# Kernel optimization log

Hardware: AMD Instinct MI355X
Metric: run time of the kernel (lower is better)

The kernel has to match this reference:

```python
import jax, jax.numpy as jnp
import numpy as np
import math

V, BS, D, L, H = 50257, 1024, 768, 12, 4
DH = D // H  # 192
B, T = 4, 1024


def setup_inputs() -> dict:
    key = jax.random.key(0)
    ks = jax.random.split(key, 18)
    s = 0.02
    inp = {
        "x": jax.random.randint(ks[0], (B, T), 0, V),
        "tok_emb": jax.random.normal(ks[1], (V, D), jnp.float32) * s,
        "pos_emb": jax.random.normal(ks[2], (BS, D), jnp.float32) * s,
        "ln1_s": jnp.ones((L, D), jnp.float32),
        "ln1_b": jnp.zeros((L, D), jnp.float32),
        "qkv_w": jax.random.normal(ks[3], (L, D, 3 * D), jnp.float32) * s,
        "qkv_b": jnp.zeros((L, 3 * D), jnp.float32),
        "ln2_s": jnp.ones((L, D), jnp.float32),
        "ln2_b": jnp.zeros((L, D), jnp.float32),
        "fc_w": jax.random.normal(ks[4], (L, D, 4 * D), jnp.float32) * s,
        "fc_b": jnp.zeros((L, 4 * D), jnp.float32),
        "proj_w": jax.random.normal(ks[5], (L, 4 * D, D), jnp.float32) * s,
        "proj_b": jnp.zeros((L, D), jnp.float32),
        "lnf_s": jnp.ones((D,), jnp.float32),
        "lnf_b": jnp.zeros((D,), jnp.float32),
        "head_w": jax.random.normal(ks[6], (D, V), jnp.float32) * s,
        "head_b": jnp.zeros((V,), jnp.float32),
    }
    return inp


def _ln(x, scale, shift):
    m = x.mean(-1, keepdims=True)
    v = jnp.mean((x - m) ** 2, axis=-1, keepdims=True)
    return (x - m) * jax.lax.rsqrt(v + 1e-5) * scale + shift


def _forward(x, tok_emb, pos_emb, ln1_s, ln1_b, qkv_w, qkv_b, ln2_s, ln2_b,
             fc_w, fc_b, proj_w, proj_b, lnf_s, lnf_b, head_w, head_b):
    Bx, Tx = x.shape
    h = tok_emb[x] + pos_emb[:Tx]  # [B,T,D]
    causal = jnp.tril(jnp.ones((Tx, Tx), bool))
    scale = 1.0 / math.sqrt(DH)

    def block(h, p):
        s1, b1, wq, bq, s2, b2, wf, bf, wp, bp = p
        # attention (no output projection, faithful to source)
        ln1 = _ln(h, s1, b1)
        qkv = ln1 @ wq + bq  # [B,T,3D]
        q, k, v = jnp.split(qkv, 3, axis=-1)
        q = q.reshape(Bx, Tx, H, DH)
        k = k.reshape(Bx, Tx, H, DH)
        v = v.reshape(Bx, Tx, H, DH)
        att = jnp.einsum('bthd,bshd->bhts', q, k) * scale
        att = jnp.where(causal, att, -jnp.inf)
        att = jax.nn.softmax(att, axis=-1)
        y = jnp.einsum('bhts,bshd->bthd', att, v).reshape(Bx, Tx, D)
        h = h + y
        # MLP (ReLU, despite attr named gelu in source)
        ln2 = _ln(h, s2, b2)
        m = jax.nn.relu(ln2 @ wf + bf) @ wp + bp
        return h + m, None

    h, _ = jax.lax.scan(block, h,
                        (ln1_s, ln1_b, qkv_w, qkv_b, ln2_s, ln2_b,
                         fc_w, fc_b, proj_w, proj_b))
    h = _ln(h, lnf_s, lnf_b)
    return h @ head_w + head_b  # [B,T,V]


def reference(x, tok_emb, pos_emb, ln1_s, ln1_b, qkv_w, qkv_b, ln2_s, ln2_b,
              fc_w, fc_b, proj_w, proj_b, lnf_s, lnf_b, head_w, head_b):
    return _forward(x, tok_emb, pos_emb, ln1_s, ln1_b, qkv_w, qkv_b,
                    ln2_s, ln2_b, fc_w, fc_b, proj_w, proj_b,
                    lnf_s, lnf_b, head_w, head_b)
```

## Files before the change

### kernel.cpp

```cpp
#include <hip/hip_runtime.h>
#include <stdint.h>

#define D_MODEL 768
#define NHEAD 4
#define DHEAD 192
#define SEQ 1024
#define NLAYER 12
#define NTOK 4096
#define NVOCAB 50257

typedef __attribute__((ext_vector_type(4))) float f32x4;
typedef __attribute__((ext_vector_type(4))) int i32x4;
typedef __attribute__((ext_vector_type(4))) unsigned short u16x4;

__device__ __forceinline__ unsigned short f2bf(float f) {
  unsigned u = __builtin_bit_cast(unsigned, f);
  u += 0x7FFFu + ((u >> 16) & 1u);
  return (unsigned short)(u >> 16);
}

#define GLDS(src, dst)                                                   \
  __builtin_amdgcn_global_load_lds(                                      \
      (const __attribute__((address_space(1))) void*)(src),              \
      (__attribute__((address_space(3))) void*)(dst), 16, 0, 0)

__global__ __launch_bounds__(256) void embed_kernel(
    const int* __restrict__ x, const float* __restrict__ tok,
    const float* __restrict__ pos, float* __restrict__ h) {
  int row = blockIdx.x;
  int t = row & (SEQ - 1);
  int id = x[row];
  const float* tp = tok + (long)id * D_MODEL;
  const float* pp = pos + (long)t * D_MODEL;
  float* hp = h + (long)row * D_MODEL;
  for (int j = threadIdx.x; j < D_MODEL; j += 256)
    hp[j] = tp[j] + pp[j];
}

__global__ __launch_bounds__(256) void ln_kernel(
    const float* __restrict__ h, const float* __restrict__ sc,
    const float* __restrict__ sh, unsigned short* __restrict__ out) {
  __shared__ float red[4];
  int row = blockIdx.x;
  const float* x = h + (long)row * D_MODEL;
  int tid = threadIdx.x;
  float v0 = x[tid], v1 = x[tid + 256], v2 = x[tid + 512];
  float s = v0 + v1 + v2;
  for (int o = 32; o > 0; o >>= 1) s += __shfl_xor(s, o);
  if ((tid & 63) == 0) red[tid >> 6] = s;
  __syncthreads();
  float mean = (red[0] + red[1] + red[2] + red[3]) * (1.0f / D_MODEL);
  __syncthreads();
  float d0 = v0 - mean, d1 = v1 - mean, d2 = v2 - mean;
  float q = d0 * d0 + d1 * d1 + d2 * d2;
  for (int o = 32; o > 0; o >>= 1) q += __shfl_xor(q, o);
  if ((tid & 63) == 0) red[tid >> 6] = q;
  __syncthreads();
  float var = (red[0] + red[1] + red[2] + red[3]) * (1.0f / D_MODEL);
  float r = rsqrtf(var + 1e-5f);
  unsigned short* op = out + (long)row * D_MODEL;
  op[tid]       = f2bf(d0 * r * sc[tid]       + sh[tid]);
  op[tid + 256] = f2bf(d1 * r * sc[tid + 256] + sh[tid + 256]);
  op[tid + 512] = f2bf(d2 * r * sc[tid + 512] + sh[tid + 512]);
}

__global__ __launch_bounds__(256) void wtrans3_kernel(
    const float* __restrict__ qw, const float* __restrict__ fw,
    const float* __restrict__ pw, unsigned short* __restrict__ tq,
    unsigned short* __restrict__ tf, unsigned short* __restrict__ tp) {
  __shared__ unsigned short tile[32][33];
  int bid = blockIdx.x;
  const float* src; unsigned short* dst; int K, N, nb;
  if (bid < 1728)               { src = qw; dst = tq; K = 768;  N = 2304; nb = 72; }
  else if ((bid -= 1728) < 2304){ src = fw; dst = tf; K = 768;  N = 3072; nb = 96; }
  else { bid -= 2304;             src = pw; dst = tp; K = 3072; N = 768;  nb = 24; }
  int n0 = (bid % nb) * 32, k0 = (bid / nb) * 32;
  int tx = threadIdx.x & 31, ty = threadIdx.x >> 5;
  #pragma unroll
  for (int i = 0; i < 4; ++i) {
    int k = k0 + ty + i * 8;
    tile[ty + i * 8][tx] = f2bf(src[(long)k * N + n0 + tx]);
  }
  __syncthreads();
  #pragma unroll
  for (int i = 0; i < 4; ++i) {
    int nn = n0 + ty + i * 8;
    dst[(long)nn * K + k0 + tx] = tile[tx][ty + i * 8];
  }
}

__global__ __launch_bounds__(256) void wtrans_kernel(
    const float* __restrict__ w, unsigned short* __restrict__ wt, int K, int N) {
  __shared__ unsigned short tile[32][33];
  int n0 = blockIdx.x * 32, k0 = blockIdx.y * 32;
  int tx = threadIdx.x, ty = threadIdx.y;
  int n = n0 + tx; if (n >= N) n = N - 1;
  #pragma unroll
  for (int i = 0; i < 4; ++i) {
    int k = k0 + ty + i * 8;
    tile[ty + i * 8][tx] = f2bf(w[(long)k * N + n]);
  }
  __syncthreads();
  #pragma unroll
  for (int i = 0; i < 4; ++i) {
    int nn = n0 + ty + i * 8;
    if (nn < N) wt[(long)nn * K + k0 + tx] = tile[tx][ty + i * 8];
  }
}

__global__ __launch_bounds__(256) void vt_kernel(
    const unsigned short* __restrict__ qkv, unsigned short* __restrict__ vt) {
  __shared__ unsigned short tile[32][33];
  int bh = blockIdx.z, b = bh >> 2, hh = bh & 3;
  int t0 = blockIdx.x * 32, f0 = blockIdx.y * 32;
  int tx = threadIdx.x, ty = threadIdx.y;
  const unsigned short* src = qkv + (long)b * SEQ * 2304 + 2 * D_MODEL + hh * DHEAD;
  #pragma unroll
  for (int i = 0; i < 4; ++i) {
    int t = t0 + ty + i * 8;
    tile[ty + i * 8][tx] = src[(long)t * 2304 + f0 + tx];
  }
  __syncthreads();
  unsigned short* dst = vt + (long)bh * DHEAD * SEQ;
  #pragma unroll
  for (int i = 0; i < 4; ++i) {
    int f = f0 + ty + i * 8;
    dst[(long)f * SEQ + t0 + tx] = tile[tx][ty + i * 8];
  }
}

__global__ __launch_bounds__(256) void softmax_kernel(
    const float* __restrict__ S, unsigned short* __restrict__ P) {
  __shared__ float red[4];
  long rid = blockIdx.x;
  int q = (int)(rid & (SEQ - 1));
  int tid = threadIdx.x;
  int i0 = tid * 4;
  f32x4 v;
  if (i0 <= q) {
    v = *(const f32x4*)(S + rid * SEQ + i0);
  } else {
    v = f32x4{-3.0e38f, -3.0e38f, -3.0e38f, -3.0e38f};
  }
  float m = -3.0e38f;
  #pragma unroll
  for (int j = 0; j < 4; ++j) {
    if (i0 + j > q) v[j] = -3.0e38f;
    m = fmaxf(m, v[j]);
  }
  for (int o = 32; o > 0; o >>= 1) m = fmaxf(m, __shfl_xor(m, o));
  if ((tid & 63) == 0) red[tid >> 6] = m;
  __syncthreads();
  m = fmaxf(fmaxf(red[0], red[1]), fmaxf(red[2], red[3]));
  __syncthreads();
  float e[4];
  float sum = 0.f;
  #pragma unroll
  for (int j = 0; j < 4; ++j) {
    e[j] = (i0 + j > q) ? 0.f : __expf(v[j] - m);
    sum += e[j];
  }
  for (int o = 32; o > 0; o >>= 1) sum += __shfl_xor(sum, o);
  if ((tid & 63) == 0) red[tid >> 6] = sum;
  __syncthreads();
  float inv = 1.0f / (red[0] + red[1] + red[2] + red[3]);
  if ((i0 >> 7) <= (q >> 7)) {
    u16x4 out;
    #pragma unroll
    for (int j = 0; j < 4; ++j) out[j] = f2bf(e[j] * inv);
    *(u16x4*)(P + rid * SEQ + i0) = out;
  }
}

#define BM 128
#define BN 128
#define BKK 32

template<int MODE>
__global__ __launch_bounds__(256) void gemm_kernel(
    const unsigned short* __restrict__ A, int lda,
    const unsigned short* __restrict__ B, int ldb,
    const float* __restrict__ bias,
    void* __restrict__ Cv, int ldc,
    int M, int N, int K,
    int NI, long sAo, long sAi, long sBo, long sBi,
    long sCo, long sCi, float alpha, int causal, int mblocks) {
  __shared__ __align__(16) unsigned short As[2][BM * BKK];
  __shared__ __align__(16) unsigned short Bs[2][BN * BKK];
  int z = blockIdx.z;
  int zo = z / NI, zi = z - zo * NI;
  A += zo * sAo + zi * sAi;
  B += zo * sBo + zi * sBi;
  long coff = zo * sCo + zi * sCi;

  int m0, n0;
  if (mblocks > 0) {
    int bid = blockIdx.x;
    int mpx = mblocks >> 3;
    int xcd = bid & 7;
    int c = bid >> 3;
    m0 = (xcd * mpx + (c & (mpx - 1))) * BM;
    n0 = (c / mpx) * BN;
  } else {
    m0 = blockIdx.y * BM;
    n0 = blockIdx.x * BN;
  }
  if (causal == 1 && n0 > m0 + BM - 1) return;
  int kmax = (causal == 2) ? min(K, m0 + BM) : K;

  int tid = threadIdx.x;
  int lane = tid & 63;
  int wave = tid >> 6;
  int wm = (wave >> 1) * 64;
  int wn = (wave & 1) * 64;

  auto stage = [&](int buf, int k0) {
    #pragma unroll
    for (int i = 0; i < 2; ++i) {
      int c0 = i * 256 + wave * 64;
      int cc = c0 + lane;
      int row = cc >> 2;
      int ko = (cc & 3) << 3;
      GLDS(A + (long)(m0 + row) * lda + k0 + ko, As[buf] + c0 * 8);
      int rg = n0 + row; if (rg >= N) rg = N - 1;
      GLDS(B + (long)rg * ldb + k0 + ko, Bs[buf] + c0 * 8);
    }
  };

  f32x4 acc[4][4] = {};
  int nt = kmax / BKK;
  stage(0, 0);
  __syncthreads();
  int cur = 0;
  for (int t = 0; t < nt; ++t) {
    if (t + 1 < nt) stage(cur ^ 1, (t + 1) * BKK);
    int lr = lane & 15;
    int kg = (lane >> 4) << 3;
    i32x4 af[4], bf[4];
    #pragma unroll
    for (int mi = 0; mi < 4; ++mi)
      af[mi] = *(const i32x4*)(As[cur] + (wm + mi * 16 + lr) * BKK + kg);
    #pragma unroll
    for (int ni = 0; ni < 4; ++ni)
      bf[ni] = *(const i32x4*)(Bs[cur] + (wn + ni * 16 + lr) * BKK + kg);
    #pragma unroll
    for (int mi = 0; mi < 4; ++mi)
      #pragma unroll
      for (int ni = 0; ni < 4; ++ni)
        asm("v_mfma_f32_16x16x32_bf16 %0, %1, %2, %0"
            : "+v"(acc[mi][ni]) : "v"(bf[ni]), "v"(af[mi]));
    __syncthreads();
    cur ^= 1;
  }

  int cm = lane & 15;
  int cg = (lane >> 4) << 2;
  #pragma unroll
  for (int mi = 0; mi < 4; ++mi) {
    long row = m0 + wm + mi * 16 + cm;
    #pragma unroll
    for (int ni = 0; ni < 4; ++ni) {
      int col = n0 + wn + ni * 16 + cg;
      f32x4 v = acc[mi][ni];
      if (MODE == 2) {
        #pragma unroll
        for (int r = 0; r < 4; ++r) v[r] *= alpha;
        *(f32x4*)((float*)Cv + coff + row * (long)ldc + col) = v;
      } else if (MODE == 0 || MODE == 1) {
        f32x4 bv = *(const f32x4*)(bias + col);
        u16x4 o;
        #pragma unroll
        for (int r = 0; r < 4; ++r) {
          float t = v[r] + bv[r];
          if (MODE == 1) t = fmaxf(t, 0.f);
          o[r] = f2bf(t);
        }
        *(u16x4*)((unsigned short*)Cv + coff + row * (long)ldc + col) = o;
      } else {
        float* cp = (float*)Cv + coff + row * (long)ldc + col;
        if (col + 4 <= N) {
          f32x4 bv = bias ? *(const f32x4*)(bias + col)
                          : f32x4{0.f, 0.f, 0.f, 0.f};
          if (MODE == 3) {
            f32x4 old = *(f32x4*)cp;
            #pragma unroll
            for (int r = 0; r < 4; ++r) old[r] += v[r] + bv[r];
            *(f32x4*)cp = old;
          } else {
            f32x4 o;
            #pragma unroll
            for (int r = 0; r < 4; ++r) o[r] = v[r] + bv[r];
            *(f32x4*)cp = o;
          }
        } else {
          #pragma unroll
          for (int r = 0; r < 4; ++r) {
            if (col + r < N) {
              float bvr = bias ? bias[col + r] : 0.f;
              if (MODE == 3) cp[r] += v[r] + bvr;
              else           cp[r] = v[r] + bvr;
            }
          }
        }
      }
    }
  }
}

extern "C" void kernel_launch(void* const* d_in, const int* in_sizes, int n_in,
                              void* d_out, int out_size, void* d_ws, size_t ws_size,
                              hipStream_t stream) {
  const int*   x       = (const int*)  d_in[0];
  const float* tok_emb = (const float*)d_in[1];
  const float* pos_emb = (const float*)d_in[2];
  const float* ln1_s   = (const float*)d_in[3];
  const float* ln1_b   = (const float*)d_in[4];
  const float* qkv_w   = (const float*)d_in[5];
  const float* qkv_b   = (const float*)d_in[6];
  const float* ln2_s   = (const float*)d_in[7];
  const float* ln2_b   = (const float*)d_in[8];
  const float* fc_w    = (const float*)d_in[9];
  const float* fc_b    = (const float*)d_in[10];
  const float* proj_w  = (const float*)d_in[11];
  const float* proj_b  = (const float*)d_in[12];
  const float* lnf_s   = (const float*)d_in[13];
  const float* lnf_b   = (const float*)d_in[14];
  const float* head_w  = (const float*)d_in[15];
  const float* head_b  = (const float*)d_in[16];

  char* ws = (char*)d_ws;
  size_t off = 0;
  auto alloc = [&](size_t bytes) {
    char* p = ws + off;
    off += (bytes + 255) & ~(size_t)255;
    return p;
  };
  float*          h   = (float*)         alloc((size_t)NTOK * D_MODEL * 4);
  unsigned short* lnb = (unsigned short*)alloc((size_t)NTOK * D_MODEL * 2);
  unsigned short* qkv = (unsigned short*)alloc((size_t)NTOK * 2304 * 2);
  unsigned short* vt  = (unsigned short*)alloc((size_t)16 * DHEAD * SEQ * 2);
  unsigned short* mid = (unsigned short*)alloc((size_t)NTOK * 3072 * 2);
  float*          S   = (float*)         alloc((size_t)16 * SEQ * SEQ * 4);
  unsigned short* P   = (unsigned short*)alloc((size_t)16 * SEQ * SEQ * 2);
  unsigned short* wtq = (unsigned short*)alloc((size_t)2304 * 768 * 2);
  unsigned short* wtf = (unsigned short*)alloc((size_t)3072 * 768 * 2);
  unsigned short* wtp = (unsigned short*)alloc((size_t)768 * 3072 * 2);
  unsigned short* wth = (unsigned short*)alloc((size_t)50304 * 768 * 2);

  embed_kernel<<<NTOK, 256, 0, stream>>>(x, tok_emb, pos_emb, h);

  const float rscale = 0.07216878364870323f;

  for (int l = 0; l < NLAYER; ++l) {
    wtrans3_kernel<<<6336, 256, 0, stream>>>(
        qkv_w + (long)l * 768 * 2304, fc_w + (long)l * 768 * 3072,
        proj_w + (long)l * 3072 * 768, wtq, wtf, wtp);
    ln_kernel<<<NTOK, 256, 0, stream>>>(h, ln1_s + l * 768, ln1_b + l * 768, lnb);
    gemm_kernel<0><<<dim3(18, 32, 1), 256, 0, stream>>>(
        lnb, 768, wtq, 768, qkv_b + l * 2304, qkv, 2304,
        4096, 2304, 768, 1, 0, 0, 0, 0, 0, 0, 1.0f, 0, 0);
    vt_kernel<<<dim3(32, 6, 16), dim3(32, 8), 0, stream>>>(qkv, vt);
    gemm_kernel<2><<<dim3(8, 8, 16), 256, 0, stream>>>(
        qkv, 2304, qkv + 768, 2304, nullptr, S, 1024,
        1024, 1024, 192, 4,
        (long)1024 * 2304, 192, (long)1024 * 2304, 192,
        (long)4 * 1024 * 1024, (long)1024 * 1024, rscale, 1, 0);
    softmax_kernel<<<16384, 256, 0, stream>>>(S, P);
    gemm_kernel<3><<<dim3(2, 8, 16), 256, 0, stream>>>(
        P, 1024, vt, 1024, nullptr, h, 768,
        1024, 192, 1024, 4,
        (long)4 * 1024 * 1024, (long)1024 * 1024,
        (long)4 * 192 * 1024, (long)192 * 1024,
        (long)1024 * 768, 192, 1.0f, 2, 0);
    ln_kernel<<<NTOK, 256, 0, stream>>>(h, ln2_s + l * 768, ln2_b + l * 768, lnb);
    gemm_kernel<1><<<dim3(24, 32, 1), 256, 0, stream>>>(
        lnb, 768, wtf, 768, fc_b + l * 3072, mid, 3072,
        4096, 3072, 768, 1, 0, 0, 0, 0, 0, 0, 1.0f, 0, 0);
    gemm_kernel<3><<<dim3(6, 32, 1), 256, 0, stream>>>(
        mid, 3072, wtp, 3072, proj_b + l * 768, h, 768,
        4096, 768, 3072, 1, 0, 0, 0, 0, 0, 0, 1.0f, 0, 0);
  }

  wtrans_kernel<<<dim3(1571, 24), dim3(32, 8), 0, stream>>>(head_w, wth, 768, 50257);
  ln_kernel<<<NTOK, 256, 0, stream>>>(h, lnf_s, lnf_b, lnb);
  gemm_kernel<4><<<dim3(32 * 393, 1, 1), 256, 0, stream>>>(
      lnb, 768, wth, 768, head_b, (float*)d_out, 50257,
      4096, 50257, 768, 1, 0, 0, 0, 0, 0, 0, 1.0f, 0, 32);
}
```

Before: 3.273 ms.

## Add 256x256 tiled bf16 MFMA GEMM for QKV, FC and LM-head matmuls

Introduces a 512-thread GEMM kernel with 256x256 output tiles, 64-wide K steps, double-buffered LDS loaded via global_load_lds with an XOR swizzle, and MFMA issue split into four phases interleaved with staging of the next tiles. Blocks are mapped XCD-aware so neighbouring M tiles share an XCD's L2. It replaces the 128x128 GEMM for the QKV, FC and vocab-head projections, aiming for more data reuse per tile and better overlap of loads with compute. The larger tile raises register and LDS pressure and gives fewer blocks for the smaller GEMMs (144 for QKV), which may leave CUs underused.

```diff
diff --git a/kernel.cpp b/kernel.cpp
--- a/kernel.cpp
+++ b/kernel.cpp
@@ -23,6 +23,14 @@
   __builtin_amdgcn_global_load_lds(                                      \
       (const __attribute__((address_space(1))) void*)(src),              \
       (__attribute__((address_space(3))) void*)(dst), 16, 0, 0)
+
+#define FENCE asm volatile("" ::: "memory")
+#define BAR()                         \
+  do {                                \
+    FENCE;                            \
+    __builtin_amdgcn_s_barrier();     \
+    FENCE;                            \
+  } while (0)
 
 __global__ __launch_bounds__(256) void embed_kernel(
     const int* __restrict__ x, const float* __restrict__ tok,
@@ -169,6 +177,192 @@
     #pragma unroll
     for (int j = 0; j < 4; ++j) out[j] = f2bf(e[j] * inv);
     *(u16x4*)(P + rid * SEQ + i0) = out;
+  }
+}
+
+
+template<int MODE>
+__global__ __launch_bounds__(512, 2) void gemm256_kernel(
+    const unsigned short* __restrict__ A,
+    const unsigned short* __restrict__ B,
+    const float* __restrict__ bias,
+    void* __restrict__ Cv, int ldc,
+    int M, int N, int K, int mb) {
+  __shared__ __align__(16) unsigned short lds[2][2][2][128 * 64];
+
+  int tid = threadIdx.x;
+  int lane = tid & 63;
+  int wid = tid >> 6;
+  int wm = wid >> 2;
+  int wn = wid & 3;
+
+  int bid = blockIdx.x;
+  int mpx = mb >> 3;
+  int xcd = bid & 7;
+  int c = bid >> 3;
+  int m0 = (xcd * mpx + (c & (mpx - 1))) * 256;
+  int n0 = (c / mpx) * 256;
+
+  auto stageA = [&](int buf, int half, int kt) {
+    const unsigned short* src = A + (long)(m0 + half * 128) * K + kt * 64;
+    #pragma unroll
+    for (int i = 0; i < 2; ++i) {
+      int chunk = i * 8 + wid;
+      int r = chunk * 8 + (lane >> 3);
+      int cc = ((lane & 7) ^ (lane >> 3)) << 3;
+      GLDS(src + (long)r * K + cc, &lds[buf][0][half][chunk * 512]);
+    }
+  };
+  auto stageB = [&](int buf, int half, int kt) {
+    #pragma unroll
+    for (int i = 0; i < 2; ++i) {
+      int chunk = i * 8 + wid;
+      int r = chunk * 8 + (lane >> 3);
+      int cc = ((lane & 7) ^ (lane >> 3)) << 3;
+      int rg = n0 + half * 128 + r;
+      if (rg >= N) rg = N - 1;
+      GLDS(B + (long)rg * K + kt * 64 + cc, &lds[buf][1][half][chunk * 512]);
+    }
+  };
+
+  auto lda_frag = [&](int buf, int f, int s) -> i32x4 {
+    int r = wm * 64 + (f & 3) * 16 + (lane & 15);
+    int kb = s * 64 + ((lane >> 4) << 4);
+    int off = r * 128 + (kb ^ ((r & 7) << 4));
+    return *(const i32x4*)((const char*)&lds[buf][0][f >> 2][0] + off);
+  };
+  auto ldb_frag = [&](int buf, int g, int s) -> i32x4 {
+    int r = wn * 32 + (g & 1) * 16 + (lane & 15);
+    int kb = s * 64 + ((lane >> 4) << 4);
+    int off = r * 128 + (kb ^ ((r & 7) << 4));
+    return *(const i32x4*)((const char*)&lds[buf][1][g >> 1][0] + off);
+  };
+
+  f32x4 acc[8][4] = {};
+  i32x4 a[4][2], b[4][2];
+
+  int nt = K / 64;
+
+  stageA(0, 0, 0); stageB(0, 0, 0); stageB(0, 1, 0); stageA(0, 1, 0);
+  stageA(1, 0, 1); stageB(1, 0, 1); stageB(1, 1, 1);
+  asm volatile("s_waitcnt vmcnt(6)" ::: "memory");
+  BAR();
+
+  for (int t = 0; t < nt; ++t) {
+    int buf = t & 1, nbuf = buf ^ 1;
+    #pragma unroll
+    for (int fi = 0; fi < 4; ++fi) {
+      a[fi][0] = lda_frag(buf, fi, 0);
+      a[fi][1] = lda_frag(buf, fi, 1);
+    }
+    #pragma unroll
+    for (int gi = 0; gi < 2; ++gi) {
+      b[gi][0] = ldb_frag(buf, gi, 0);
+      b[gi][1] = ldb_frag(buf, gi, 1);
+    }
+    if (t + 1 < nt) stageA(nbuf, 1, t + 1);
+    BAR();
+    __builtin_amdgcn_s_setprio(1);
+    #pragma unroll
+    for (int s = 0; s < 2; ++s)
+      #pragma unroll
+      for (int fi = 0; fi < 4; ++fi)
+        #pragma unroll
+        for (int gi = 0; gi < 2; ++gi)
+          asm("v_mfma_f32_16x16x32_bf16 %0, %1, %2, %0"
+              : "+v"(acc[fi][gi]) : "v"(b[gi][s]), "v"(a[fi][s]));
+    __builtin_amdgcn_s_setprio(0);
+    BAR();
+    #pragma unroll
+    for (int gi = 2; gi < 4; ++gi) {
+      b[gi][0] = ldb_frag(buf, gi, 0);
+      b[gi][1] = ldb_frag(buf, gi, 1);
+    }
+    if (t + 2 < nt) stageA(buf, 0, t + 2);
+    BAR();
+    __builtin_amdgcn_s_setprio(1);
+    #pragma unroll
+    for (int s = 0; s < 2; ++s)
+      #pragma unroll
+      for (int fi = 0; fi < 4; ++fi)
+        #pragma unroll
+        for (int gi = 2; gi < 4; ++gi)
+          asm("v_mfma_f32_16x16x32_bf16 %0, %1, %2, %0"
+              : "+v"(acc[fi][gi]) : "v"(b[gi][s]), "v"(a[fi][s]));
+    __builtin_amdgcn_s_setprio(0);
+    BAR();
+    #pragma unroll
+    for (int fi = 0; fi < 4; ++fi) {
+      a[fi][0] = lda_frag(buf, 4 + fi, 0);
+      a[fi][1] = lda_frag(buf, 4 + fi, 1);
+    }
+    if (t + 2 < nt) stageB(buf, 0, t + 2);
+    BAR();
+    __builtin_amdgcn_s_setprio(1);
+    #pragma unroll
+    for (int s = 0; s < 2; ++s)
+      #pragma unroll
+      for (int fi = 0; fi < 4; ++fi)
+        #pragma unroll
+        for (int gi = 2; gi < 4; ++gi)
+          asm("v_mfma_f32_16x16x32_bf16 %0, %1, %2, %0"
+              : "+v"(acc[4 + fi][gi]) : "v"(b[gi][s]), "v"(a[fi][s]));
+    __builtin_amdgcn_s_setprio(0);
+    BAR();
+    if (t + 2 < nt) {
+      stageB(buf, 1, t + 2);
+      asm volatile("s_waitcnt vmcnt(6)" ::: "memory");
+    } else if (t + 1 < nt) {
+      asm volatile("s_waitcnt vmcnt(0)" ::: "memory");
+    }
+    BAR();
+    __builtin_amdgcn_s_setprio(1);
+    #pragma unroll
+    for (int s = 0; s < 2; ++s)
+      #pragma unroll
+      for (int fi = 0; fi < 4; ++fi)
+        #pragma unroll
+        for (int gi = 0; gi < 2; ++gi)
+          asm("v_mfma_f32_16x16x32_bf16 %0, %1, %2, %0"
+              : "+v"(acc[4 + fi][gi]) : "v"(b[gi][s]), "v"(a[fi][s]));
+    __builtin_amdgcn_s_setprio(0);
+    BAR();
+  }
+
+  int cr = lane & 15;
+  int cg = (lane >> 4) << 2;
+  #pragma unroll
+  for (int f = 0; f < 8; ++f) {
+    long row = m0 + wm * 64 + (f & 3) * 16 + (f >> 2) * 128 + cr;
+    #pragma unroll
+    for (int g = 0; g < 4; ++g) {
+      int col = n0 + wn * 32 + (g & 1) * 16 + (g >> 1) * 128 + cg;
+      f32x4 v = acc[f][g];
+      if (MODE == 0 || MODE == 1) {
+        f32x4 bv = *(const f32x4*)(bias + col);
+        u16x4 o;
+        #pragma unroll
+        for (int r = 0; r < 4; ++r) {
+          float tt = v[r] + bv[r];
+          if (MODE == 1) tt = fmaxf(tt, 0.f);
+          o[r] = f2bf(tt);
+        }
+        *(u16x4*)((unsigned short*)Cv + row * (long)ldc + col) = o;
+      } else {
+        float* cp = (float*)Cv + row * (long)ldc + col;
+        if (col + 4 <= N) {
+          f32x4 bv = *(const f32x4*)(bias + col);
+          f32x4 o;
+          #pragma unroll
+          for (int r = 0; r < 4; ++r) o[r] = v[r] + bv[r];
+          *(f32x4*)cp = o;
+        } else {
+          #pragma unroll
+          for (int r = 0; r < 4; ++r)
+            if (col + r < N) cp[r] = v[r] + bias[col + r];
+        }
+      }
+    }
   }
 }
 
@@ -356,9 +550,8 @@
         qkv_w + (long)l * 768 * 2304, fc_w + (long)l * 768 * 3072,
         proj_w + (long)l * 3072 * 768, wtq, wtf, wtp);
     ln_kernel<<<NTOK, 256, 0, stream>>>(h, ln1_s + l * 768, ln1_b + l * 768, lnb);
-    gemm_kernel<0><<<dim3(18, 32, 1), 256, 0, stream>>>(
-        lnb, 768, wtq, 768, qkv_b + l * 2304, qkv, 2304,
-        4096, 2304, 768, 1, 0, 0, 0, 0, 0, 0, 1.0f, 0, 0);
+    gemm256_kernel<0><<<16 * 9, 512, 0, stream>>>(
+        lnb, wtq, qkv_b + l * 2304, qkv, 2304, 4096, 2304, 768, 16);
     vt_kernel<<<dim3(32, 6, 16), dim3(32, 8), 0, stream>>>(qkv, vt);
     gemm_kernel<2><<<dim3(8, 8, 16), 256, 0, stream>>>(
         qkv, 2304, qkv + 768, 2304, nullptr, S, 1024,
@@ -373,9 +566,8 @@
         (long)4 * 192 * 1024, (long)192 * 1024,
         (long)1024 * 768, 192, 1.0f, 2, 0);
     ln_kernel<<<NTOK, 256, 0, stream>>>(h, ln2_s + l * 768, ln2_b + l * 768, lnb);
-    gemm_kernel<1><<<dim3(24, 32, 1), 256, 0, stream>>>(
-        lnb, 768, wtf, 768, fc_b + l * 3072, mid, 3072,
-        4096, 3072, 768, 1, 0, 0, 0, 0, 0, 0, 1.0f, 0, 0);
+    gemm256_kernel<1><<<16 * 12, 512, 0, stream>>>(
+        lnb, wtf, fc_b + l * 3072, mid, 3072, 4096, 3072, 768, 16);
     gemm_kernel<3><<<dim3(6, 32, 1), 256, 0, stream>>>(
         mid, 3072, wtp, 3072, proj_b + l * 768, h, 768,
         4096, 768, 3072, 1, 0, 0, 0, 0, 0, 0, 1.0f, 0, 0);
@@ -383,7 +575,6 @@
 
   wtrans_kernel<<<dim3(1571, 24), dim3(32, 8), 0, stream>>>(head_w, wth, 768, 50257);
   ln_kernel<<<NTOK, 256, 0, stream>>>(h, lnf_s, lnf_b, lnb);
-  gemm_kernel<4><<<dim3(32 * 393, 1, 1), 256, 0, stream>>>(
-      lnb, 768, wth, 768, head_b, (float*)d_out, 50257,
-      4096, 50257, 768, 1, 0, 0, 0, 0, 0, 0, 1.0f, 0, 32);
-}
+  gemm256_kernel<4><<<16 * 197, 512, 0, stream>>>(
+      lnb, wth, head_b, (float*)d_out, 50257, 4096, 50257, 768, 16);
+}
```

Result: no change. 3.213 ms (-1.8%).
